# Optimization experiments

Hardware: AMD Instinct MI355X
Metric: run time of the kernel (lower is better)

The kernel has to match this reference:

```python
import jax, jax.numpy as jnp
import numpy as np

N_NODES = 50000
N_EDGES = 1600000
D = 128
NUM_GRAPHS = 64


def gcn_conv(x, src, dst, ew, W, b, n):
    # PyG GCNConv: add self-loops (weight 1), symmetric normalization,
    # message = norm * (x @ W)[src], aggregated at dst, then + bias.
    loop = jnp.arange(n)
    src2 = jnp.concatenate([src, loop])
    dst2 = jnp.concatenate([dst, loop])
    ew2 = jnp.concatenate([ew, jnp.ones((n,), dtype=x.dtype)])
    deg = jax.ops.segment_sum(ew2, dst2, num_segments=n)  # [N]
    dinv = jnp.where(deg > 0, jax.lax.rsqrt(deg), 0.0)
    norm = dinv[src2] * ew2 * dinv[dst2]                  # [E+N]
    xw = x @ W                                            # [N, out]
    msg = xw[src2] * norm[:, None]                        # [E+N, out]
    return jax.ops.segment_sum(msg, dst2, num_segments=n) + b


def setup_inputs() -> dict:
    key = jax.random.key(0)
    ks = jax.random.split(key, 10)
    x = jax.random.normal(ks[0], (N_NODES, D), dtype=jnp.float32)
    edge_index = jax.random.randint(ks[1], (2, N_EDGES), 0, N_NODES, dtype=jnp.int32)
    edge_weight = jax.random.uniform(ks[2], (N_EDGES,), dtype=jnp.float32)
    batch = jnp.sort(jax.random.randint(ks[3], (N_NODES,), 0, NUM_GRAPHS, dtype=jnp.int32))
    s = 1.0 / np.sqrt(D)
    W0 = jax.random.uniform(ks[4], (D, D), jnp.float32, -s, s)
    W1 = jax.random.uniform(ks[5], (D, D), jnp.float32, -s, s)
    W2 = jax.random.uniform(ks[6], (D, D), jnp.float32, -s, s)
    b0 = jnp.zeros((D,), jnp.float32)
    b1 = jnp.zeros((D,), jnp.float32)
    b2 = jnp.zeros((D,), jnp.float32)
    return {"x": x, "edge_index": edge_index, "edge_weight": edge_weight,
            "batch": batch, "W0": W0, "b0": b0, "W1": W1, "b1": b1,
            "W2": W2, "b2": b2}


def reference(x, edge_index, edge_weight, batch, W0, b0, W1, b1, W2, b2):
    src, dst = edge_index[0], edge_index[1]
    n = x.shape[0]
    h = gcn_conv(x, src, dst, edge_weight, W0, b0, n)
    h = jax.nn.relu(h)  # dropout=0.0 (eval)
    h = gcn_conv(h, src, dst, edge_weight, W1, b1, n)
    h = jax.nn.relu(h)
    h = gcn_conv(h, src, dst, edge_weight, W2, b2, n)
    # global mean pool over graphs in the batch
    sums = jax.ops.segment_sum(h, batch, num_segments=NUM_GRAPHS)
    cnts = jax.ops.segment_sum(jnp.ones((n,), h.dtype), batch, num_segments=NUM_GRAPHS)
    return sums / jnp.maximum(cnts, 1.0)[:, None]
```

## Files before the change

### kernel.cpp

```cpp
#include <hip/hip_runtime.h>
#include <hip/hip_fp16.h>


#define DFEAT 128
#define BLK_E 4096
#define NPART 8

typedef _Float16 half8 __attribute__((ext_vector_type(8)));
typedef float floatx4 __attribute__((ext_vector_type(4)));

__device__ __forceinline__ int wave_incl_scan(int v) {
    int incl = v;
    #pragma unroll
    for (int off = 1; off < 64; off <<= 1) {
        int u = __shfl_up(incl, (unsigned)off, 64);
        if ((int)(threadIdx.x & 63) >= off) incl += u;
    }
    return incl;
}

__device__ __forceinline__ void wconv_elem(int idx, const float* __restrict__ W0,
                                           const float* __restrict__ W1,
                                           const float* __restrict__ W2,
                                           _Float16* __restrict__ Wsw) {
    if (idx >= 3 * 128 * 128) return;
    int w = idx >> 14;
    int r = idx & 16383;
    int k = r >> 7, nn = r & 127;
    const float* W = (w == 0) ? W0 : (w == 1) ? W1 : W2;
    float v = W[k * 128 + nn];
    _Float16 hi = (_Float16)v;
    _Float16 lo = (_Float16)((v - (float)hi) * 1024.0f);
    int kk = k >> 5, quad = (k >> 3) & 3, j = k & 7;
    int t = nn >> 4, L = quad * 16 + (nn & 15);
    int off = ((kk * 8 + t) * 64 + L) * 8 + j;
    Wsw[(size_t)(w * 2 + 0) * 16384 + off] = hi;
    Wsw[(size_t)(w * 2 + 1) * 16384 + off] = lo;
}

__global__ __launch_bounds__(256) void hist_k(const int* __restrict__ dst,
                                              int* __restrict__ hist,
                                              const float* __restrict__ W0,
                                              const float* __restrict__ W1,
                                              const float* __restrict__ W2,
                                              _Float16* __restrict__ Wsw,
                                              float* __restrict__ out,
                                              float* __restrict__ pool_cnt,
                                              int E, int nblk, int nbuck) {
    __shared__ int h[256];
    int tid = threadIdx.x, b = blockIdx.x;
    h[tid] = 0;
    if (b < 48) {
        #pragma unroll
        for (int k = 0; k < 4; k++)
            wconv_elem(b * 1024 + k * 256 + tid, W0, W1, W2, Wsw);
    }
    if (b < 8) {
        floatx4 z = {0.f, 0.f, 0.f, 0.f};
        ((floatx4*)out)[b * 256 + tid] = z;
    }
    if (b == 8 && tid < 64) pool_cnt[tid] = 0.f;
    __syncthreads();
    int base = b * BLK_E;
    int nE = min(BLK_E, E - base);
    for (int i = tid; i < nE; i += 256) atomicAdd(&h[dst[base + i] >> 8], 1);
    __syncthreads();
    if (tid < nbuck) hist[tid * nblk + b] = h[tid];
}

__global__ __launch_bounds__(256) void scanb_k(int* __restrict__ arr,
                                               int* __restrict__ blksum,
                                               int n_val, int n_scan) {
    int tid = threadIdx.x;
    int base = blockIdx.x * 1024 + tid * 4;
    int v0 = (base + 0 < n_val) ? arr[base + 0] : 0;
    int v1 = (base + 1 < n_val) ? arr[base + 1] : 0;
    int v2 = (base + 2 < n_val) ? arr[base + 2] : 0;
    int v3 = (base + 3 < n_val) ? arr[base + 3] : 0;
    int tsum = v0 + v1 + v2 + v3;
    int incl = wave_incl_scan(tsum);
    __shared__ int wtot[4];
    if ((tid & 63) == 63) wtot[tid >> 6] = incl;
    __syncthreads();
    int woff = 0;
    for (int w = 0; w < (tid >> 6); w++) woff += wtot[w];
    int texcl = woff + incl - tsum;
    if (base + 0 < n_scan) arr[base + 0] = texcl;
    if (base + 1 < n_scan) arr[base + 1] = texcl + v0;
    if (base + 2 < n_scan) arr[base + 2] = texcl + v0 + v1;
    if (base + 3 < n_scan) arr[base + 3] = texcl + v0 + v1 + v2;
    if (tid == 255) blksum[blockIdx.x] = woff + incl;
}

__global__ __launch_bounds__(256) void scan_small256(int* __restrict__ blksum, int nb) {
    int tid = threadIdx.x;
    int v = (tid < nb) ? blksum[tid] : 0;
    int incl = wave_incl_scan(v);
    __shared__ int wtot[4];
    if ((tid & 63) == 63) wtot[tid >> 6] = incl;
    __syncthreads();
    int woff = 0;
    for (int w = 0; w < (tid >> 6); w++) woff += wtot[w];
    if (tid < nb) blksum[tid] = woff + incl - v;
}

__global__ __launch_bounds__(512) void scat_k(const int* __restrict__ src,
                                              const int* __restrict__ dst,
                                              const float* __restrict__ ew,
                                              const int* __restrict__ offs,
                                              const int* __restrict__ blksum,
                                              uint2* __restrict__ rec,
                                              int E, int nblk, int nbuck) {
    __shared__ int lcur[256];
    __shared__ int gbase[256];
    __shared__ uint2 srec[BLK_E];
    __shared__ int gpos[BLK_E];
    __shared__ int wtot[4];
    int tid = threadIdx.x, b = blockIdx.x;
    if (tid < 256) lcur[tid] = 0;
    __syncthreads();
    int base = b * BLK_E;
    int nE = min(BLK_E, E - base);
    for (int i = tid; i < nE; i += 512) atomicAdd(&lcur[dst[base + i] >> 8], 1);
    __syncthreads();
    int v = 0, incl = 0;
    if (tid < 256) { v = lcur[tid]; incl = wave_incl_scan(v); }
    if (tid < 256 && (tid & 63) == 63) wtot[tid >> 6] = incl;
    __syncthreads();
    if (tid < 256) {
        int woff = 0;
        for (int w = 0; w < (tid >> 6); w++) woff += wtot[w];
        int excl = woff + incl - v;
        lcur[tid] = excl;
        int oidx = tid * nblk + b;
        gbase[tid] = (tid < nbuck) ? (offs[oidx] + blksum[oidx >> 10] - excl) : 0;
    }
    __syncthreads();
    for (int i = tid; i < nE; i += 512) {
        int e = base + i;
        int d = dst[e];
        int bin = d >> 8;
        int slot = atomicAdd(&lcur[bin], 1);
        uint2 r;
        r.x = (unsigned)src[e] | ((unsigned)(d & 255) << 16);
        r.y = __float_as_uint(ew[e]);
        srec[slot] = r;
        gpos[slot] = gbase[bin] + slot;
    }
    __syncthreads();
    for (int i = tid; i < nE; i += 512) rec[gpos[i]] = srec[i];
}

__global__ __launch_bounds__(1024) void bucket_k(const uint2* __restrict__ rec,
                                                 const int* __restrict__ offs,
                                                 const int* __restrict__ blksum,
                                                 float* __restrict__ dinv,
                                                 int* __restrict__ rp8,
                                                 unsigned* __restrict__ csr,
                                                 int N, int nblk) {
    __shared__ int cnt[2048];
    __shared__ unsigned degfx[256];
    __shared__ int cur[2048];
    __shared__ int wtot[16];
    int tid = threadIdx.x, bin = blockIdx.x;
    int idx0 = bin * nblk, idx1 = (bin + 1) * nblk;
    int start = offs[idx0] + blksum[idx0 >> 10];
    int endp  = offs[idx1] + blksum[idx1 >> 10];
    cnt[tid] = 0; cnt[tid + 1024] = 0;
    if (tid < 256) degfx[tid] = 0;
    __syncthreads();
    for (int i = start + tid; i < endp; i += 1024) {
        uint2 r = rec[i];
        int dl = (r.x >> 16) & 255;
        int part = (r.x & 0xffff) >> 13;
        atomicAdd(&cnt[dl * NPART + part], 1);
        atomicAdd(&degfx[dl], (unsigned)(__uint_as_float(r.y) * 1048576.0f + 0.5f));
    }
    __syncthreads();
    int v0 = cnt[tid * 2], v1 = cnt[tid * 2 + 1];
    int tsum = v0 + v1;
    int incl = wave_incl_scan(tsum);
    if ((tid & 63) == 63) wtot[tid >> 6] = incl;
    __syncthreads();
    int woff = 0;
    for (int w = 0; w < (tid >> 6); w++) woff += wtot[w];
    int texcl = woff + incl - tsum;
    cur[tid * 2] = texcl;
    cur[tid * 2 + 1] = texcl + v0;
    rp8[bin * 2048 + tid * 2] = start + texcl;
    rp8[bin * 2048 + tid * 2 + 1] = start + texcl + v0;
    __syncthreads();
    if (tid < 256) {
        int node = bin * 256 + tid;
        if (node < N) {
            float deg = (float)degfx[tid] * (1.0f / 1048576.0f) + 1.0f;
            float di = rsqrtf(deg);
            dinv[node] = di;
            degfx[tid] = __float_as_uint(di);
        }
    }
    __syncthreads();
    for (int i = start + tid; i < endp; i += 1024) {
        uint2 r = rec[i];
        int dl = (r.x >> 16) & 255;
        int s = r.x & 0xffff;
        int part = s >> 13;
        int p = start + atomicAdd(&cur[dl * NPART + part], 1);
        float di_d = __uint_as_float(degfx[dl]);
        float nm = __uint_as_float(r.y) * di_d;
        unsigned h = (unsigned)__half_as_ushort(__float2half_rn(nm));
        csr[p] = (unsigned)s | (h << 16);
    }
}

__global__ __launch_bounds__(512) void gemm_mfma(const _Float16* __restrict__ A,
                                                 const _Float16* __restrict__ Wsw,
                                                 const float* __restrict__ dinv,
                                                 _Float16* __restrict__ C, int n) {
    __shared__ _Float16 Bl[2 * 16384];
    {
        const uint4* s = (const uint4*)Wsw;
        uint4* d = (uint4*)Bl;
        for (int i = threadIdx.x; i < 4096; i += 512) d[i] = s[i];
    }
    int wave = threadIdx.x >> 6, lane = threadIdx.x & 63;
    int quad = lane >> 4, mcol = lane & 15;
    int row0 = blockIdx.x * 128 + wave * 16 + mcol;
    half8 af[4] = {};
    if (row0 < n) {
        const half8* Arow = (const half8*)(A + (size_t)row0 * DFEAT);
        af[0] = Arow[0 + quad];
        af[1] = Arow[4 + quad];
        af[2] = Arow[8 + quad];
        af[3] = Arow[12 + quad];
    }
    __syncthreads();
    floatx4 acch[8] = {};
    floatx4 accl[8] = {};
    const half8* Bh = (const half8*)Bl;
    const half8* Blo = (const half8*)(Bl + 16384);
    #pragma unroll
    for (int kk = 0; kk < 4; kk++) {
        #pragma unroll
        for (int t = 0; t < 8; t++) {
            half8 bh = Bh[(kk * 8 + t) * 64 + lane];
            acch[t] = __builtin_amdgcn_mfma_f32_16x16x32_f16(af[kk], bh, acch[t], 0, 0, 0);
            half8 bl = Blo[(kk * 8 + t) * 64 + lane];
            accl[t] = __builtin_amdgcn_mfma_f32_16x16x32_f16(af[kk], bl, accl[t], 0, 0, 0);
        }
    }
    int orow_base = blockIdx.x * 128 + wave * 16 + quad * 4;
    float dv[4];
    #pragma unroll
    for (int r = 0; r < 4; r++)
        dv[r] = (orow_base + r < n) ? dinv[orow_base + r] : 0.f;
    #pragma unroll
    for (int t = 0; t < 8; t++) {
        #pragma unroll
        for (int r = 0; r < 4; r++) {
            int orow = orow_base + r;
            if (orow < n) {
                float v = (acch[t][r] + accl[t][r] * (1.0f / 1024.0f)) * dv[r];
                C[(size_t)orow * DFEAT + t * 16 + mcol] = (_Float16)v;
            }
        }
    }
}

__global__ __launch_bounds__(512) void gemm_mfma_f32(const float* __restrict__ A,
                                                     const _Float16* __restrict__ Wsw,
                                                     const float* __restrict__ dinv,
                                                     _Float16* __restrict__ C, int n) {
    __shared__ _Float16 Bl[2 * 16384];
    {
        const uint4* s = (const uint4*)Wsw;
        uint4* d = (uint4*)Bl;
        for (int i = threadIdx.x; i < 4096; i += 512) d[i] = s[i];
    }
    int wave = threadIdx.x >> 6, lane = threadIdx.x & 63;
    int quad = lane >> 4, mcol = lane & 15;
    int row0 = blockIdx.x * 128 + wave * 16 + mcol;
    half8 af[4] = {};
    if (row0 < n) {
        const float4* Arow = (const float4*)(A + (size_t)row0 * DFEAT);
        #pragma unroll
        for (int kk = 0; kk < 4; kk++) {
            float4 f0 = Arow[kk * 8 + quad * 2];
            float4 f1 = Arow[kk * 8 + quad * 2 + 1];
            half8 a;
            a[0] = (_Float16)f0.x; a[1] = (_Float16)f0.y;
            a[2] = (_Float16)f0.z; a[3] = (_Float16)f0.w;
            a[4] = (_Float16)f1.x; a[5] = (_Float16)f1.y;
            a[6] = (_Float16)f1.z; a[7] = (_Float16)f1.w;
            af[kk] = a;
        }
    }
    __syncthreads();
    floatx4 acch[8] = {};
    floatx4 accl[8] = {};
    const half8* Bh = (const half8*)Bl;
    const half8* Blo = (const half8*)(Bl + 16384);
    #pragma unroll
    for (int kk = 0; kk < 4; kk++) {
        #pragma unroll
        for (int t = 0; t < 8; t++) {
            half8 bh = Bh[(kk * 8 + t) * 64 + lane];
            acch[t] = __builtin_amdgcn_mfma_f32_16x16x32_f16(af[kk], bh, acch[t], 0, 0, 0);
            half8 bl = Blo[(kk * 8 + t) * 64 + lane];
            accl[t] = __builtin_amdgcn_mfma_f32_16x16x32_f16(af[kk], bl, accl[t], 0, 0, 0);
        }
    }
    int orow_base = blockIdx.x * 128 + wave * 16 + quad * 4;
    float dv[4];
    #pragma unroll
    for (int r = 0; r < 4; r++)
        dv[r] = (orow_base + r < n) ? dinv[orow_base + r] : 0.f;
    #pragma unroll
    for (int t = 0; t < 8; t++) {
        #pragma unroll
        for (int r = 0; r < 4; r++) {
            int orow = orow_base + r;
            if (orow < n) {
                float v = (acch[t][r] + accl[t][r] * (1.0f / 1024.0f)) * dv[r];
                C[(size_t)orow * DFEAT + t * 16 + mcol] = (_Float16)v;
            }
        }
    }
}

__global__ __launch_bounds__(256) void agg_k(const __half2* __restrict__ xw2,
                                             const int* __restrict__ rp8,
                                             const unsigned* __restrict__ csr,
                                             const float* __restrict__ dinv,
                                             const float* __restrict__ bias,
                                             __half2* __restrict__ out, int relu, int n) {
    int node = blockIdx.x * 4 + (threadIdx.x >> 6);
    if (node >= n) return;
    int lane = threadIdx.x & 63;
    float di = dinv[node];
    float2 selfv = __half22float2(xw2[(size_t)node * 64 + lane]);
    float ax = di * selfv.x, ay = di * selfv.y;
    int e = rp8[node * NPART], end = rp8[node * NPART + NPART];
    for (; e + 4 <= end; e += 4) {
        unsigned c0 = csr[e + 0], c1 = csr[e + 1];
        unsigned c2 = csr[e + 2], c3 = csr[e + 3];
        float2 v0 = __half22float2(xw2[(size_t)(c0 & 0xffff) * 64 + lane]);
        float2 v1 = __half22float2(xw2[(size_t)(c1 & 0xffff) * 64 + lane]);
        float2 v2 = __half22float2(xw2[(size_t)(c2 & 0xffff) * 64 + lane]);
        float2 v3 = __half22float2(xw2[(size_t)(c3 & 0xffff) * 64 + lane]);
        float w0 = __half2float(__ushort_as_half((unsigned short)(c0 >> 16)));
        float w1 = __half2float(__ushort_as_half((unsigned short)(c1 >> 16)));
        float w2 = __half2float(__ushort_as_half((unsigned short)(c2 >> 16)));
        float w3 = __half2float(__ushort_as_half((unsigned short)(c3 >> 16)));
        ax = fmaf(w0, v0.x, ax); ay = fmaf(w0, v0.y, ay);
        ax = fmaf(w1, v1.x, ax); ay = fmaf(w1, v1.y, ay);
        ax = fmaf(w2, v2.x, ax); ay = fmaf(w2, v2.y, ay);
        ax = fmaf(w3, v3.x, ax); ay = fmaf(w3, v3.y, ay);
    }
    for (; e < end; e++) {
        unsigned c = csr[e];
        float w = __half2float(__ushort_as_half((unsigned short)(c >> 16)));
        float2 v = __half22float2(xw2[(size_t)(c & 0xffff) * 64 + lane]);
        ax = fmaf(w, v.x, ax); ay = fmaf(w, v.y, ay);
    }
    float2 bv = ((const float2*)bias)[lane];
    ax += bv.x; ay += bv.y;
    if (relu) { ax = fmaxf(ax, 0.f); ay = fmaxf(ay, 0.f); }
    out[(size_t)node * 64 + lane] = __floats2half2_rn(ax, ay);
}

__global__ __launch_bounds__(128) void pool_k(const __half* __restrict__ h,
                                              const int* __restrict__ batch,
                                              float* __restrict__ out,
                                              float* __restrict__ pool_cnt, int n) {
    int j = threadIdx.x;
    int start = blockIdx.x * 64;
    if (start >= n) return;
    int end = start + 64; if (end > n) end = n;
    int g = batch[start];
    float acc = 0.f;
    float ccnt = 0.f;
    for (int i = start; i < end; i++) {
        int bi = batch[i];
        if (bi != g) {
            atomicAdd(&out[g * DFEAT + j], acc);
            if (j == 0) atomicAdd(&pool_cnt[g], ccnt);
            acc = 0.f; ccnt = 0.f; g = bi;
        }
        acc += __half2float(h[(size_t)i * DFEAT + j]);
        ccnt += 1.f;
    }
    atomicAdd(&out[g * DFEAT + j], acc);
    if (j == 0) atomicAdd(&pool_cnt[g], ccnt);
}

__global__ void div_k(float* __restrict__ out, const float* __restrict__ cnt) {
    int idx = blockIdx.x * 256 + threadIdx.x;
    if (idx < 64 * DFEAT) {
        float c = cnt[idx >> 7];
        out[idx] = out[idx] / fmaxf(c, 1.0f);
    }
}

extern "C" void kernel_launch(void* const* d_in, const int* in_sizes, int n_in,
                              void* d_out, int out_size, void* d_ws, size_t ws_size,
                              hipStream_t stream) {
    const float* x    = (const float*)d_in[0];
    const int*  eidx  = (const int*)d_in[1];
    const float* ew   = (const float*)d_in[2];
    const int*  batch = (const int*)d_in[3];
    const float* W0 = (const float*)d_in[4];
    const float* b0 = (const float*)d_in[5];
    const float* W1 = (const float*)d_in[6];
    const float* b1 = (const float*)d_in[7];
    const float* W2 = (const float*)d_in[8];
    const float* b2 = (const float*)d_in[9];
    float* out = (float*)d_out;

    const int N = in_sizes[0] / DFEAT;
    const int E = in_sizes[2];
    const int* src = eidx;
    const int* dst = eidx + E;

    const int nbuck = (N + 255) / 256;
    const int nblk  = (E + BLK_E - 1) / BLK_E;
    const int total = nbuck * nblk;
    const int n_scan = total + 1;

    size_t off = 0;
    auto walloc = [&](size_t bytes) -> void* {
        void* p = (char*)d_ws + off;
        off += (bytes + 255) & ~(size_t)255;
        return p;
    };
    float*   dinv    = (float*)  walloc((size_t)N * 4);
    int*     rp8     = (int*)    walloc(((size_t)nbuck * 2048 + 8) * 4);
    int*     offs    = (int*)    walloc((size_t)n_scan * 4);
    int*     blksum  = (int*)    walloc(256 * 4);
    uint2*   rec     = (uint2*)  walloc((size_t)E * 8);
    unsigned* csr    = (unsigned*)walloc((size_t)E * 4);
    _Float16* xwH    = (_Float16*)walloc((size_t)N * DFEAT * 2);
    _Float16* hH     = (_Float16*)walloc((size_t)N * DFEAT * 2);
    _Float16* Wsw    = (_Float16*)walloc((size_t)6 * 16384 * 2);
    float*   pool_cnt= (float*)  walloc(64 * 4);

    hist_k<<<nblk, 256, 0, stream>>>(dst, offs, W0, W1, W2, Wsw, out, pool_cnt,
                                     E, nblk, nbuck);
    int nsb = (n_scan + 1023) / 1024;
    scanb_k<<<nsb, 256, 0, stream>>>(offs, blksum, total, n_scan);
    scan_small256<<<1, 256, 0, stream>>>(blksum, nsb);
    scat_k<<<nblk, 512, 0, stream>>>(src, dst, ew, offs, blksum, rec, E, nblk, nbuck);
    bucket_k<<<nbuck, 1024, 0, stream>>>(rec, offs, blksum, dinv, rp8, csr, N, nblk);

    int gG = (N + 127) / 128;
    int gA = (N + 3) / 4;
    gemm_mfma_f32<<<gG, 512, 0, stream>>>(x, Wsw + (size_t)0 * 32768, dinv, xwH, N);
    agg_k<<<gA, 256, 0, stream>>>((const __half2*)xwH, rp8, csr, dinv, b0,
                                  (__half2*)hH, 1, N);
    gemm_mfma<<<gG, 512, 0, stream>>>(hH, Wsw + (size_t)1 * 32768, dinv, xwH, N);
    agg_k<<<gA, 256, 0, stream>>>((const __half2*)xwH, rp8, csr, dinv, b1,
                                  (__half2*)hH, 1, N);
    gemm_mfma<<<gG, 512, 0, stream>>>(hH, Wsw + (size_t)2 * 32768, dinv, xwH, N);
    agg_k<<<gA, 256, 0, stream>>>((const __half2*)xwH, rp8, csr, dinv, b2,
                                  (__half2*)hH, 0, N);

    pool_k<<<(N + 63) / 64, 128, 0, stream>>>((const __half*)hH, batch, out, pool_cnt, N);
    div_k<<<32, 256, 0, stream>>>(out, pool_cnt);
}
```

Before: 373.2 us.

## Fold small scan and division kernels into neighbors, unroll aggregation by eight

Drops the separate blksum scan launch: the scan now covers 2048 entries per block, and each consumer (scat_k, bucket_k) rescans the few block sums in shared memory. Graph boundaries are found from the sorted batch array so per-graph inverse counts are known before pooling, which lets pool_k scale its partial sums directly and removes the div_k launch. The aggregation loop gains an 8-wide unrolled gather so more loads are in flight. The cost is redundant tiny scans in every block and a reliance on batch being sorted.

```diff
diff --git a/kernel.cpp b/kernel.cpp
--- a/kernel.cpp
+++ b/kernel.cpp
@@ -45,7 +45,6 @@
                                               const float* __restrict__ W2,
                                               _Float16* __restrict__ Wsw,
                                               float* __restrict__ out,
-                                              float* __restrict__ pool_cnt,
                                               int E, int nblk, int nbuck) {
     __shared__ int h[256];
     int tid = threadIdx.x, b = blockIdx.x;
@@ -59,7 +58,6 @@
         floatx4 z = {0.f, 0.f, 0.f, 0.f};
         ((floatx4*)out)[b * 256 + tid] = z;
     }
-    if (b == 8 && tid < 64) pool_cnt[tid] = 0.f;
     __syncthreads();
     int base = b * BLK_E;
     int nE = min(BLK_E, E - base);
@@ -70,38 +68,38 @@
 
 __global__ __launch_bounds__(256) void scanb_k(int* __restrict__ arr,
                                                int* __restrict__ blksum,
-                                               int n_val, int n_scan) {
+                                               const int* __restrict__ batch,
+                                               int* __restrict__ gend,
+                                               int n_val, int n_scan,
+                                               int N, int ngraph) {
     int tid = threadIdx.x;
-    int base = blockIdx.x * 1024 + tid * 4;
-    int v0 = (base + 0 < n_val) ? arr[base + 0] : 0;
-    int v1 = (base + 1 < n_val) ? arr[base + 1] : 0;
-    int v2 = (base + 2 < n_val) ? arr[base + 2] : 0;
-    int v3 = (base + 3 < n_val) ? arr[base + 3] : 0;
-    int tsum = v0 + v1 + v2 + v3;
+    int base = blockIdx.x * 2048 + tid * 8;
+    int v[8], tsum = 0;
+    #pragma unroll
+    for (int j = 0; j < 8; j++) {
+        v[j] = (base + j < n_val) ? arr[base + j] : 0;
+        tsum += v[j];
+    }
     int incl = wave_incl_scan(tsum);
     __shared__ int wtot[4];
     if ((tid & 63) == 63) wtot[tid >> 6] = incl;
     __syncthreads();
     int woff = 0;
     for (int w = 0; w < (tid >> 6); w++) woff += wtot[w];
-    int texcl = woff + incl - tsum;
-    if (base + 0 < n_scan) arr[base + 0] = texcl;
-    if (base + 1 < n_scan) arr[base + 1] = texcl + v0;
-    if (base + 2 < n_scan) arr[base + 2] = texcl + v0 + v1;
-    if (base + 3 < n_scan) arr[base + 3] = texcl + v0 + v1 + v2;
+    int run = woff + incl - tsum;
+    #pragma unroll
+    for (int j = 0; j < 8; j++) {
+        if (base + j < n_scan) arr[base + j] = run;
+        run += v[j];
+    }
     if (tid == 255) blksum[blockIdx.x] = woff + incl;
-}
-
-__global__ __launch_bounds__(256) void scan_small256(int* __restrict__ blksum, int nb) {
-    int tid = threadIdx.x;
-    int v = (tid < nb) ? blksum[tid] : 0;
-    int incl = wave_incl_scan(v);
-    __shared__ int wtot[4];
-    if ((tid & 63) == 63) wtot[tid >> 6] = incl;
-    __syncthreads();
-    int woff = 0;
-    for (int w = 0; w < (tid >> 6); w++) woff += wtot[w];
-    if (tid < nb) blksum[tid] = woff + incl - v;
+    int stride = gridDim.x * 256;
+    for (int i = blockIdx.x * 256 + tid; i < N; i += stride) {
+        int b0 = batch[i];
+        int b1 = (i + 1 < N) ? batch[i + 1] : ngraph;
+        if (i == 0) for (int g = 0; g < b0; g++) gend[g] = 0;
+        if (b0 != b1) for (int g = b0; g < b1; g++) gend[g] = i + 1;
+    }
 }
 
 __global__ __launch_bounds__(512) void scat_k(const int* __restrict__ src,
@@ -109,15 +107,32 @@
                                               const float* __restrict__ ew,
                                               const int* __restrict__ offs,
                                               const int* __restrict__ blksum,
+                                              const int* __restrict__ gend,
+                                              float* __restrict__ pool_inv,
                                               uint2* __restrict__ rec,
-                                              int E, int nblk, int nbuck) {
+                                              int E, int nblk, int nbuck,
+                                              int nsb, int ngraph) {
     __shared__ int lcur[256];
     __shared__ int gbase[256];
     __shared__ uint2 srec[BLK_E];
     __shared__ int gpos[BLK_E];
     __shared__ int wtot[4];
+    __shared__ int bsc[64];
     int tid = threadIdx.x, b = blockIdx.x;
     if (tid < 256) lcur[tid] = 0;
+    if (tid >= 256 && tid < 320) {
+        int t = tid - 256;
+        int v = (t < nsb) ? blksum[t] : 0;
+        int incl = wave_incl_scan(v);
+        bsc[t] = incl - v;
+    }
+    if (b == 0 && tid >= 320 && tid < 384) {
+        int t = tid - 320;
+        if (t < ngraph) {
+            int c = gend[t] - (t ? gend[t - 1] : 0);
+            pool_inv[t] = 1.0f / fmaxf((float)c, 1.0f);
+        }
+    }
     __syncthreads();
     int base = b * BLK_E;
     int nE = min(BLK_E, E - base);
@@ -133,7 +148,7 @@
         int excl = woff + incl - v;
         lcur[tid] = excl;
         int oidx = tid * nblk + b;
-        gbase[tid] = (tid < nbuck) ? (offs[oidx] + blksum[oidx >> 10] - excl) : 0;
+        gbase[tid] = (tid < nbuck) ? (offs[oidx] + bsc[oidx >> 11] - excl) : 0;
     }
     __syncthreads();
     for (int i = tid; i < nE; i += 512) {
@@ -157,18 +172,25 @@
                                                  float* __restrict__ dinv,
                                                  int* __restrict__ rp8,
                                                  unsigned* __restrict__ csr,
-                                                 int N, int nblk) {
+                                                 int N, int nblk, int nsb) {
     __shared__ int cnt[2048];
     __shared__ unsigned degfx[256];
     __shared__ int cur[2048];
     __shared__ int wtot[16];
+    __shared__ int bsc[64];
     int tid = threadIdx.x, bin = blockIdx.x;
-    int idx0 = bin * nblk, idx1 = (bin + 1) * nblk;
-    int start = offs[idx0] + blksum[idx0 >> 10];
-    int endp  = offs[idx1] + blksum[idx1 >> 10];
     cnt[tid] = 0; cnt[tid + 1024] = 0;
     if (tid < 256) degfx[tid] = 0;
-    __syncthreads();
+    if (tid >= 256 && tid < 320) {
+        int t = tid - 256;
+        int v = (t < nsb) ? blksum[t] : 0;
+        int incl = wave_incl_scan(v);
+        bsc[t] = incl - v;
+    }
+    __syncthreads();
+    int idx0 = bin * nblk, idx1 = (bin + 1) * nblk;
+    int start = offs[idx0] + bsc[idx0 >> 11];
+    int endp  = offs[idx1] + bsc[idx1 >> 11];
     for (int i = start + tid; i < endp; i += 1024) {
         uint2 r = rec[i];
         int dl = (r.x >> 16) & 255;
@@ -341,6 +363,36 @@
     float2 selfv = __half22float2(xw2[(size_t)node * 64 + lane]);
     float ax = di * selfv.x, ay = di * selfv.y;
     int e = rp8[node * NPART], end = rp8[node * NPART + NPART];
+    for (; e + 8 <= end; e += 8) {
+        unsigned c0 = csr[e + 0], c1 = csr[e + 1];
+        unsigned c2 = csr[e + 2], c3 = csr[e + 3];
+        unsigned c4 = csr[e + 4], c5 = csr[e + 5];
+        unsigned c6 = csr[e + 6], c7 = csr[e + 7];
+        float2 v0 = __half22float2(xw2[(size_t)(c0 & 0xffff) * 64 + lane]);
+        float2 v1 = __half22float2(xw2[(size_t)(c1 & 0xffff) * 64 + lane]);
+        float2 v2 = __half22float2(xw2[(size_t)(c2 & 0xffff) * 64 + lane]);
+        float2 v3 = __half22float2(xw2[(size_t)(c3 & 0xffff) * 64 + lane]);
+        float2 v4 = __half22float2(xw2[(size_t)(c4 & 0xffff) * 64 + lane]);
+        float2 v5 = __half22float2(xw2[(size_t)(c5 & 0xffff) * 64 + lane]);
+        float2 v6 = __half22float2(xw2[(size_t)(c6 & 0xffff) * 64 + lane]);
+        float2 v7 = __half22float2(xw2[(size_t)(c7 & 0xffff) * 64 + lane]);
+        float w0 = __half2float(__ushort_as_half((unsigned short)(c0 >> 16)));
+        float w1 = __half2float(__ushort_as_half((unsigned short)(c1 >> 16)));
+        float w2 = __half2float(__ushort_as_half((unsigned short)(c2 >> 16)));
+        float w3 = __half2float(__ushort_as_half((unsigned short)(c3 >> 16)));
+        float w4 = __half2float(__ushort_as_half((unsigned short)(c4 >> 16)));
+        float w5 = __half2float(__ushort_as_half((unsigned short)(c5 >> 16)));
+        float w6 = __half2float(__ushort_as_half((unsigned short)(c6 >> 16)));
+        float w7 = __half2float(__ushort_as_half((unsigned short)(c7 >> 16)));
+        ax = fmaf(w0, v0.x, ax); ay = fmaf(w0, v0.y, ay);
+        ax = fmaf(w1, v1.x, ax); ay = fmaf(w1, v1.y, ay);
+        ax = fmaf(w2, v2.x, ax); ay = fmaf(w2, v2.y, ay);
+        ax = fmaf(w3, v3.x, ax); ay = fmaf(w3, v3.y, ay);
+        ax = fmaf(w4, v4.x, ax); ay = fmaf(w4, v4.y, ay);
+        ax = fmaf(w5, v5.x, ax); ay = fmaf(w5, v5.y, ay);
+        ax = fmaf(w6, v6.x, ax); ay = fmaf(w6, v6.y, ay);
+        ax = fmaf(w7, v7.x, ax); ay = fmaf(w7, v7.y, ay);
+    }
     for (; e + 4 <= end; e += 4) {
         unsigned c0 = csr[e + 0], c1 = csr[e + 1];
         unsigned c2 = csr[e + 2], c3 = csr[e + 3];
@@ -372,34 +424,22 @@
 __global__ __launch_bounds__(128) void pool_k(const __half* __restrict__ h,
                                               const int* __restrict__ batch,
                                               float* __restrict__ out,
-                                              float* __restrict__ pool_cnt, int n) {
+                                              const float* __restrict__ pool_inv, int n) {
     int j = threadIdx.x;
     int start = blockIdx.x * 64;
     if (start >= n) return;
     int end = start + 64; if (end > n) end = n;
     int g = batch[start];
     float acc = 0.f;
-    float ccnt = 0.f;
     for (int i = start; i < end; i++) {
         int bi = batch[i];
         if (bi != g) {
-            atomicAdd(&out[g * DFEAT + j], acc);
-            if (j == 0) atomicAdd(&pool_cnt[g], ccnt);
-            acc = 0.f; ccnt = 0.f; g = bi;
+            atomicAdd(&out[g * DFEAT + j], acc * pool_inv[g]);
+            acc = 0.f; g = bi;
         }
         acc += __half2float(h[(size_t)i * DFEAT + j]);
-        ccnt += 1.f;
-    }
-    atomicAdd(&out[g * DFEAT + j], acc);
-    if (j == 0) atomicAdd(&pool_cnt[g], ccnt);
-}
-
-__global__ void div_k(float* __restrict__ out, const float* __restrict__ cnt) {
-    int idx = blockIdx.x * 256 + threadIdx.x;
-    if (idx < 64 * DFEAT) {
-        float c = cnt[idx >> 7];
-        out[idx] = out[idx] / fmaxf(c, 1.0f);
-    }
+    }
+    atomicAdd(&out[g * DFEAT + j], acc * pool_inv[g]);
 }
 
 extern "C" void kernel_launch(void* const* d_in, const int* in_sizes, int n_in,
@@ -419,6 +459,7 @@
 
     const int N = in_sizes[0] / DFEAT;
     const int E = in_sizes[2];
+    const int ngraph = out_size / DFEAT;
     const int* src = eidx;
     const int* dst = eidx + E;
 
@@ -426,6 +467,7 @@
     const int nblk  = (E + BLK_E - 1) / BLK_E;
     const int total = nbuck * nblk;
     const int n_scan = total + 1;
+    const int nsb = (n_scan + 2047) / 2048;
 
     size_t off = 0;
     auto walloc = [&](size_t bytes) -> void* {
@@ -442,15 +484,17 @@
     _Float16* xwH    = (_Float16*)walloc((size_t)N * DFEAT * 2);
     _Float16* hH     = (_Float16*)walloc((size_t)N * DFEAT * 2);
     _Float16* Wsw    = (_Float16*)walloc((size_t)6 * 16384 * 2);
-    float*   pool_cnt= (float*)  walloc(64 * 4);
-
-    hist_k<<<nblk, 256, 0, stream>>>(dst, offs, W0, W1, W2, Wsw, out, pool_cnt,
+    float*   pool_inv= (float*)  walloc(64 * 4);
+    int*     gend    = (int*)    walloc(64 * 4);
+
+    hist_k<<<nblk, 256, 0, stream>>>(dst, offs, W0, W1, W2, Wsw, out,
                                      E, nblk, nbuck);
-    int nsb = (n_scan + 1023) / 1024;
-    scanb_k<<<nsb, 256, 0, stream>>>(offs, blksum, total, n_scan);
-    scan_small256<<<1, 256, 0, stream>>>(blksum, nsb);
-    scat_k<<<nblk, 512, 0, stream>>>(src, dst, ew, offs, blksum, rec, E, nblk, nbuck);
-    bucket_k<<<nbuck, 1024, 0, stream>>>(rec, offs, blksum, dinv, rp8, csr, N, nblk);
+    scanb_k<<<nsb, 256, 0, stream>>>(offs, blksum, batch, gend, total, n_scan,
+                                     N, ngraph);
+    scat_k<<<nblk, 512, 0, stream>>>(src, dst, ew, offs, blksum, gend, pool_inv,
+                                     rec, E, nblk, nbuck, nsb, ngraph);
+    bucket_k<<<nbuck, 1024, 0, stream>>>(rec, offs, blksum, dinv, rp8, csr,
+                                         N, nblk, nsb);
 
     int gG = (N + 127) / 128;
     int gA = (N + 3) / 4;
@@ -464,6 +508,6 @@
     agg_k<<<gA, 256, 0, stream>>>((const __half2*)xwH, rp8, csr, dinv, b2,
                                   (__half2*)hH, 0, N);
 
-    pool_k<<<(N + 63) / 64, 128, 0, stream>>>((const __half*)hH, batch, out, pool_cnt, N);
-    div_k<<<32, 256, 0, stream>>>(out, pool_cnt);
-}
+    pool_k<<<(N + 63) / 64, 128, 0, stream>>>((const __half*)hH, batch, out,
+                                              pool_inv, N);
+}
```

Measured after the change: 344.6 us. -7.7%, faster.
